# Kernel optimization log

Hardware: AMD Instinct MI355X
Metric: run time of the kernel (lower is better)

## Reference

```python
import jax, jax.numpy as jnp
import numpy as np

H = W = 256
WS = 8      # window size
SS = 4      # shift size
NH = 3      # num heads
EPS = 1e-5


def _rel_pos_index(ws):
    coords = np.stack(np.meshgrid(np.arange(ws), np.arange(ws), indexing='ij')).reshape(2, -1)
    rel = (coords[:, :, None] - coords[:, None, :]).transpose(1, 2, 0)
    rel[..., 0] += ws - 1
    rel[..., 1] += ws - 1
    rel[..., 0] *= 2 * ws - 1
    return rel.sum(-1)  # (ws*ws, ws*ws) int


def _attn_mask(h, w, ws, ss):
    img = np.zeros((h, w))
    cnt = 0
    for hs in (slice(0, -ws), slice(-ws, -ss), slice(-ss, None)):
        for wsl in (slice(0, -ws), slice(-ws, -ss), slice(-ss, None)):
            img[hs, wsl] = cnt
            cnt += 1
    mw = img.reshape(h // ws, ws, w // ws, ws).transpose(0, 2, 1, 3).reshape(-1, ws * ws)
    am = mw[:, None, :] - mw[:, :, None]
    return np.where(am != 0, -100.0, 0.0).astype(np.float32)  # (nW, N, N)


_RPI = jnp.asarray(_rel_pos_index(WS))
_MASK = jnp.asarray(_attn_mask(H, W, WS, SS))


def _ln(x, w, b):
    m = x.mean(-1, keepdims=True)
    v = ((x - m) ** 2).mean(-1, keepdims=True)
    return (x - m) * jax.lax.rsqrt(v + EPS) * w + b


def setup_inputs() -> dict:
    key = jax.random.key(0)
    ks = jax.random.split(key, 6)
    C, DFF = 96, 384
    return {
        'x': jax.random.normal(ks[0], (8, H * W, C), jnp.float32),
        'norm1_w': jnp.ones((C,), jnp.float32),
        'norm1_b': jnp.zeros((C,), jnp.float32),
        'qkv_w': jax.random.normal(ks[1], (3 * C, C), jnp.float32) * 0.02,
        'qkv_b': jnp.zeros((3 * C,), jnp.float32),
        'rpb_table': jax.random.normal(ks[2], ((2 * WS - 1) ** 2, NH), jnp.float32) * 0.02,
        'proj_w': jax.random.normal(ks[3], (C, C), jnp.float32) * 0.02,
        'proj_b': jnp.zeros((C,), jnp.float32),
        'norm2_w': jnp.ones((C,), jnp.float32),
        'norm2_b': jnp.zeros((C,), jnp.float32),
        'mlp_w1': jax.random.normal(ks[4], (DFF, C), jnp.float32) * 0.02,
        'mlp_b1': jnp.zeros((DFF,), jnp.float32),
        'mlp_w2': jax.random.normal(ks[5], (C, DFF), jnp.float32) * 0.02,
        'mlp_b2': jnp.zeros((C,), jnp.float32),
    }


def reference(x, norm1_w, norm1_b, qkv_w, qkv_b, rpb_table, proj_w, proj_b,
              norm2_w, norm2_b, mlp_w1, mlp_b1, mlp_w2, mlp_b2):
    B, L, C = x.shape
    N = WS * WS
    hd = C // NH
    scale = hd ** -0.5

    shortcut = x
    h = _ln(x, norm1_w, norm1_b).reshape(B, H, W, C)
    h = jnp.roll(h, (-SS, -SS), axis=(1, 2))
    # window partition -> (B_ , N, C)
    xw = h.reshape(B, H // WS, WS, W // WS, WS, C).transpose(0, 1, 3, 2, 4, 5).reshape(-1, N, C)
    B_ = xw.shape[0]

    qkv = (xw @ qkv_w.T + qkv_b).reshape(B_, N, 3, NH, hd).transpose(2, 0, 3, 1, 4)
    q, k, v = qkv[0], qkv[1], qkv[2]  # each (B_, NH, N, hd)
    attn = jnp.einsum('bhnd,bhmd->bhnm', q, k) * scale

    bias = rpb_table[_RPI.reshape(-1)].reshape(N, N, NH).transpose(2, 0, 1)  # (NH,N,N)
    attn = attn + bias[None]

    nW = _MASK.shape[0]
    attn = attn.reshape(B_ // nW, nW, NH, N, N) + _MASK[None, :, None]
    attn = jax.nn.softmax(attn.reshape(B_, NH, N, N), axis=-1)

    o = jnp.einsum('bhnm,bhmd->bhnd', attn, v).transpose(0, 2, 1, 3).reshape(B_, N, C)
    o = o @ proj_w.T + proj_b
    # window reverse -> (B, H, W, C)
    o = o.reshape(B, H // WS, W // WS, WS, WS, C).transpose(0, 1, 3, 2, 4, 5).reshape(B, H, W, C)
    o = jnp.roll(o, (SS, SS), axis=(1, 2))

    x1 = shortcut + o.reshape(B, L, C)
    h2 = _ln(x1, norm2_w, norm2_b)
    h2 = jax.nn.gelu(h2 @ mlp_w1.T + mlp_b1, approximate=False) @ mlp_w2.T + mlp_b2
    return x1 + h2
```

## Files before the change

kernel.cpp:

```cpp
#include <hip/hip_runtime.h>
#include <math.h>

#define HH    256
#define WWID  256
#define WSZ   8
#define SSZ   4
#define NHEAD 3
#define CCH   96
#define DFF   384

#define XW_LD 104
#define QK_LD 200
#define VT_LD 72
#define H_LD  200

using bf16x8 = __attribute__((ext_vector_type(8))) short;
using f32x4  = __attribute__((ext_vector_type(4))) float;
using int2v  = __attribute__((ext_vector_type(2))) int;

#define LOG2E 1.44269504088896f

__device__ __forceinline__ unsigned short f2bf(float f) {
    unsigned u = __float_as_uint(f);
    return (unsigned short)((u + 0x7FFFu + ((u >> 16) & 1u)) >> 16);
}
__device__ __forceinline__ float bf2f(unsigned short s) {
    return __uint_as_float(((unsigned)s) << 16);
}
__device__ __forceinline__ unsigned cvtpk(float lo, float hi) {
    unsigned r;
    asm("v_cvt_pk_bf16_f32 %0, %1, %2" : "=v"(r) : "v"(lo), "v"(hi));
    return r;
}
__device__ __forceinline__ float lo2f(unsigned u) { return __uint_as_float(u << 16); }
__device__ __forceinline__ float hi2f(unsigned u) { return __uint_as_float(u & 0xFFFF0000u); }

__device__ __forceinline__ float gelu_t(float t) {
    float t2 = t * t;
    float u  = t * (0.7978845608028654f + 0.03567740814183f * t2);
    float e  = exp2f(u * 2.885390081777927f);
    float rc = __builtin_amdgcn_rcpf(e + 1.f);
    return t - t * rc;
}

#define WQ_OFF  0
#define WP_OFF  27648
#define W1_OFF  36864
#define W2_OFF  73728
#define CT_OFF  110592

__global__ void __launch_bounds__(256)
prep(const float* __restrict__ qkvw, const float* __restrict__ pw,
     const float* __restrict__ w1, const float* __restrict__ w2,
     const float* __restrict__ rpb, unsigned short* __restrict__ wsq)
{
    int e = blockIdx.x * 256 + threadIdx.x;
    if (e < 110592) {
        const float* W; int Kd, nk, i = e;
        if (i < 27648)      { W = qkvw; Kd = 96;  nk = 3;  }
        else if (i < 36864) { W = pw;   Kd = 96;  nk = 3;  i -= 27648; }
        else if (i < 73728) { W = w1;   Kd = 96;  nk = 3;  i -= 36864; }
        else                { W = w2;   Kd = 384; nk = 12; i -= 73728; }
        int j = i & 7, fe = i >> 3;
        int lane = fe & 63, q = fe >> 6;
        int ks = q % nk, t = q / nk;
        int row = t * 16 + (lane & 15);
        int col = ks * 32 + (lane >> 4) * 8 + j;
        wsq[e] = f2bf(W[(size_t)row * Kd + col]);
    } else if (e < 159744) {
        int i = e - 110592;
        int cls = i / 12288;
        int rem = i - cls * 12288;
        int h = rem >> 12, n = (rem >> 6) & 63, m = rem & 63;
        int rel = ((n >> 3) - (m >> 3) + 7) * 15 + ((n & 7) - (m & 7) + 7);
        float bias = rpb[rel * NHEAD + h];
        int ci = cls >> 1, cj = cls & 1;
        int rn = (ci ? ((n >> 3) < 4 ? 1 : 2) : 0) * 3 + (cj ? ((n & 7) < 4 ? 1 : 2) : 0);
        int rm = (ci ? ((m >> 3) < 4 ? 1 : 2) : 0) * 3 + (cj ? ((m & 7) < 4 ? 1 : 2) : 0);
        float mask = (rn != rm) ? -100.f : 0.f;
        wsq[CT_OFF + i] = f2bf((bias + mask) * LOG2E);
    }
}

__global__ void __launch_bounds__(256, 3)
fused(const float* __restrict__ x,
      const float* __restrict__ n1w, const float* __restrict__ n1b,
      const float* __restrict__ qkvb, const float* __restrict__ pb,
      const float* __restrict__ n2w, const float* __restrict__ n2b,
      const float* __restrict__ b1, const float* __restrict__ b2,
      const unsigned short* __restrict__ wsq,
      float* __restrict__ y)
{
    __shared__ unsigned short SM[19712];
    unsigned short* sR1 = SM;
    unsigned short* sQK = SM + 6912;

    const int bwin = blockIdx.x;
    const int b  = bwin >> 10;
    const int wi = (bwin >> 5) & 31;
    const int wj = bwin & 31;
    const int tid = threadIdx.x;
    const int lane = tid & 63;
    const int wave = tid >> 6;
    const int l15 = lane & 15;
    const int l16 = lane >> 4;
    const int nb = wave * 16;
    const int sub = lane & 3;

    const int tm  = nb + (lane >> 2);
    const int gh1 = ((wi << 3) + (tm >> 3) + SSZ) & (HH - 1);
    const int gw1 = ((wj << 3) + (tm & 7) + SSZ) & (WWID - 1);
    const size_t rowtm = ((size_t)b * (HH * WWID) + (size_t)gh1 * WWID + gw1) * CCH;

    f32x4 xv[6];
    {
        const float* xr = x + rowtm + sub * 24;
#pragma unroll
        for (int q = 0; q < 6; ++q) xv[q] = *(const f32x4*)(xr + 4 * q);
        float s1 = 0.f, s2 = 0.f;
#pragma unroll
        for (int q = 0; q < 6; ++q)
#pragma unroll
            for (int r = 0; r < 4; ++r) { s1 += xv[q][r]; s2 = fmaf(xv[q][r], xv[q][r], s2); }
        s1 += __shfl_xor(s1, 1);  s2 += __shfl_xor(s2, 1);
        s1 += __shfl_xor(s1, 2);  s2 += __shfl_xor(s2, 2);
        const float mean = s1 * (1.f / CCH);
        const float rstd = rsqrtf(s2 * (1.f / CCH) - mean * mean + 1e-5f);
        unsigned o[12];
#pragma unroll
        for (int q = 0; q < 6; ++q) {
            const f32x4 wv = *(const f32x4*)&n1w[sub * 24 + 4 * q];
            const f32x4 bv = *(const f32x4*)&n1b[sub * 24 + 4 * q];
            float a0 = (xv[q][0] - mean) * rstd * wv[0] + bv[0];
            float a1 = (xv[q][1] - mean) * rstd * wv[1] + bv[1];
            float a2 = (xv[q][2] - mean) * rstd * wv[2] + bv[2];
            float a3 = (xv[q][3] - mean) * rstd * wv[3] + bv[3];
            o[2 * q] = cvtpk(a0, a1); o[2 * q + 1] = cvtpk(a2, a3);
        }
        unsigned* dst = (unsigned*)&sR1[tm * XW_LD + sub * 24];
#pragma unroll
        for (int q = 0; q < 3; ++q) {
            uint4 u; u.x = o[4 * q]; u.y = o[4 * q + 1]; u.z = o[4 * q + 2]; u.w = o[4 * q + 3];
            *(uint4*)(dst + 4 * q) = u;
        }
    }
    __syncthreads();

    bf16x8 afr[4][3];
#pragma unroll
    for (int mt = 0; mt < 4; ++mt)
#pragma unroll
        for (int ks = 0; ks < 3; ++ks)
            afr[mt][ks] = *(const bf16x8*)&sR1[(mt * 16 + l15) * XW_LD + ks * 32 + l16 * 8];
    __syncthreads();

    {
        const float qscale = 0.17677669529663689f * LOG2E;
        for (int nt = wave; nt < 18; nt += 4) {
            f32x4 acc[4] = {{0,0,0,0},{0,0,0,0},{0,0,0,0},{0,0,0,0}};
#pragma unroll
            for (int ks = 0; ks < 3; ++ks) {
                const bf16x8 wf = *(const bf16x8*)(wsq + ((size_t)(nt * 3 + ks) * 64 + lane) * 8);
#pragma unroll
                for (int mt = 0; mt < 4; ++mt)
                    acc[mt] = __builtin_amdgcn_mfma_f32_16x16x32_bf16(wf, afr[mt][ks], acc[mt], 0, 0, 0);
            }
            const f32x4 bias = *(const f32x4*)&qkvb[nt * 16 + 4 * l16];
            if (nt < 6) {
#pragma unroll
                for (int mt = 0; mt < 4; ++mt) {
                    uint2 u;
                    u.x = cvtpk((acc[mt][0] + bias[0]) * qscale, (acc[mt][1] + bias[1]) * qscale);
                    u.y = cvtpk((acc[mt][2] + bias[2]) * qscale, (acc[mt][3] + bias[3]) * qscale);
                    *(uint2*)&sQK[(mt * 16 + l15) * QK_LD + nt * 16 + 4 * l16] = u;
                }
            } else if (nt < 12) {
#pragma unroll
                for (int mt = 0; mt < 4; ++mt) {
                    uint2 u;
                    u.x = cvtpk(acc[mt][0] + bias[0], acc[mt][1] + bias[1]);
                    u.y = cvtpk(acc[mt][2] + bias[2], acc[mt][3] + bias[3]);
                    *(uint2*)&sQK[(mt * 16 + l15) * QK_LD + nt * 16 + 4 * l16] = u;
                }
            } else {
                const int ch = nt * 16 - 192 + 4 * l16;
#pragma unroll
                for (int mt = 0; mt < 4; ++mt) {
                    const unsigned v01 = cvtpk(acc[mt][0] + bias[0], acc[mt][1] + bias[1]);
                    const unsigned v23 = cvtpk(acc[mt][2] + bias[2], acc[mt][3] + bias[3]);
                    sR1[(ch + 0) * VT_LD + mt * 16 + l15] = (unsigned short)v01;
                    sR1[(ch + 1) * VT_LD + mt * 16 + l15] = (unsigned short)(v01 >> 16);
                    sR1[(ch + 2) * VT_LD + mt * 16 + l15] = (unsigned short)v23;
                    sR1[(ch + 3) * VT_LD + mt * 16 + l15] = (unsigned short)(v23 >> 16);
                }
            }
        }
    }
    __syncthreads();

    {
        const int cls = ((wi == 31) ? 2 : 0) + ((wj == 31) ? 1 : 0);
        const unsigned short* ctb = wsq + CT_OFF + cls * 12288;
        const bool godd = (l16 & 1) != 0;
#pragma unroll 1
        for (int h = 0; h < NHEAD; ++h) {
            const bf16x8 qf = *(const bf16x8*)&sQK[(nb + l15) * QK_LD + h * 32 + l16 * 8];
            f32x4 s[4];
#pragma unroll
            for (int mt = 0; mt < 4; ++mt) {
                const bf16x8 kf = *(const bf16x8*)&sQK[(mt * 16 + l15) * QK_LD + CCH + h * 32 + l16 * 8];
                f32x4 z = {0, 0, 0, 0};
                s[mt] = __builtin_amdgcn_mfma_f32_16x16x32_bf16(kf, qf, z, 0, 0, 0);
            }
            const unsigned short* cth = ctb + h * 4096 + (nb + l15) * 64;
            unsigned u[4][2];
            float rsum = 0.f;
#pragma unroll
            for (int mt = 0; mt < 4; ++mt) {
                const ushort4 c4 = *(const ushort4*)&cth[mt * 16 + 4 * l16];
                const float pv0 = exp2f(s[mt][0] + bf2f(c4.x));
                const float pv1 = exp2f(s[mt][1] + bf2f(c4.y));
                const float pv2 = exp2f(s[mt][2] + bf2f(c4.z));
                const float pv3 = exp2f(s[mt][3] + bf2f(c4.w));
                rsum += pv0 + pv1 + pv2 + pv3;
                u[mt][0] = cvtpk(pv0, pv1);
                u[mt][1] = cvtpk(pv2, pv3);
            }
            rsum += __shfl_xor(rsum, 16);
            rsum += __shfl_xor(rsum, 32);
            const float rinv = __builtin_amdgcn_rcpf(rsum);
            f32x4 o[2] = {{0,0,0,0},{0,0,0,0}};
#pragma unroll
            for (int ks = 0; ks < 2; ++ks) {
                const int2v r0 = __builtin_amdgcn_permlane32_swap(
                    (int)u[2 * ks][0], (int)u[2 * ks + 1][0], false, false);
                const int2v r1 = __builtin_amdgcn_permlane32_swap(
                    (int)u[2 * ks][1], (int)u[2 * ks + 1][1], false, false);
                const unsigned X0 = (unsigned)r0[0], Y0 = (unsigned)r0[1];
                const unsigned X1 = (unsigned)r1[0], Y1 = (unsigned)r1[1];
                const unsigned SX0 = (unsigned)__builtin_amdgcn_ds_swizzle((int)X0, 0x401F);
                const unsigned SX1 = (unsigned)__builtin_amdgcn_ds_swizzle((int)X1, 0x401F);
                const unsigned SY0 = (unsigned)__builtin_amdgcn_ds_swizzle((int)Y0, 0x401F);
                const unsigned SY1 = (unsigned)__builtin_amdgcn_ds_swizzle((int)Y1, 0x401F);
                union { unsigned w[4]; bf16x8 v; } pk;
                pk.w[0] = godd ? SY0 : X0;
                pk.w[1] = godd ? SY1 : X1;
                pk.w[2] = godd ? Y0 : SX0;
                pk.w[3] = godd ? Y1 : SX1;
#pragma unroll
                for (int dt = 0; dt < 2; ++dt) {
                    const bf16x8 vf = *(const bf16x8*)&sR1[(h * 32 + dt * 16 + l15) * VT_LD + ks * 32 + l16 * 8];
                    o[dt] = __builtin_amdgcn_mfma_f32_16x16x32_bf16(vf, pk.v, o[dt], 0, 0, 0);
                }
            }
#pragma unroll
            for (int dt = 0; dt < 2; ++dt) {
                uint2 uo;
                uo.x = cvtpk(o[dt][0] * rinv, o[dt][1] * rinv);
                uo.y = cvtpk(o[dt][2] * rinv, o[dt][3] * rinv);
                *(uint2*)&sQK[(nb + l15) * QK_LD + h * 32 + dt * 16 + 4 * l16] = uo;
            }
        }
    }
    __syncthreads();

    {
        bf16x8 ofr[4][3];
#pragma unroll
        for (int mt = 0; mt < 4; ++mt)
#pragma unroll
            for (int ks = 0; ks < 3; ++ks)
                ofr[mt][ks] = *(const bf16x8*)&sQK[(mt * 16 + l15) * QK_LD + ks * 32 + l16 * 8];
        const unsigned short* wp = wsq + WP_OFF;
        for (int ct = wave; ct < 6; ct += 4) {
            f32x4 acc[4] = {{0,0,0,0},{0,0,0,0},{0,0,0,0},{0,0,0,0}};
#pragma unroll
            for (int ks = 0; ks < 3; ++ks) {
                const bf16x8 wf = *(const bf16x8*)(wp + ((size_t)(ct * 3 + ks) * 64 + lane) * 8);
#pragma unroll
                for (int mt = 0; mt < 4; ++mt)
                    acc[mt] = __builtin_amdgcn_mfma_f32_16x16x32_bf16(wf, ofr[mt][ks], acc[mt], 0, 0, 0);
            }
            const f32x4 pbv = *(const f32x4*)&pb[ct * 16 + 4 * l16];
#pragma unroll
            for (int mt = 0; mt < 4; ++mt) {
                uint2 u;
                u.x = cvtpk(acc[mt][0] + pbv[0], acc[mt][1] + pbv[1]);
                u.y = cvtpk(acc[mt][2] + pbv[2], acc[mt][3] + pbv[3]);
                *(uint2*)&sR1[(mt * 16 + l15) * XW_LD + ct * 16 + 4 * l16] = u;
            }
        }
    }
    __syncthreads();

    float y1tm[6][4];
    {
        const unsigned* src = (const unsigned*)&sR1[tm * XW_LD + sub * 24];
#pragma unroll
        for (int q3 = 0; q3 < 3; ++q3) {
            const uint4 u = *(const uint4*)(src + 4 * q3);
            y1tm[2 * q3][0]     = xv[2 * q3][0] + lo2f(u.x);
            y1tm[2 * q3][1]     = xv[2 * q3][1] + hi2f(u.x);
            y1tm[2 * q3][2]     = xv[2 * q3][2] + lo2f(u.y);
            y1tm[2 * q3][3]     = xv[2 * q3][3] + hi2f(u.y);
            y1tm[2 * q3 + 1][0] = xv[2 * q3 + 1][0] + lo2f(u.z);
            y1tm[2 * q3 + 1][1] = xv[2 * q3 + 1][1] + hi2f(u.z);
            y1tm[2 * q3 + 1][2] = xv[2 * q3 + 1][2] + lo2f(u.w);
            y1tm[2 * q3 + 1][3] = xv[2 * q3 + 1][3] + hi2f(u.w);
        }
        float s1 = 0.f, s2 = 0.f;
#pragma unroll
        for (int q = 0; q < 6; ++q)
#pragma unroll
            for (int r = 0; r < 4; ++r) { s1 += y1tm[q][r]; s2 = fmaf(y1tm[q][r], y1tm[q][r], s2); }
        s1 += __shfl_xor(s1, 1);  s2 += __shfl_xor(s2, 1);
        s1 += __shfl_xor(s1, 2);  s2 += __shfl_xor(s2, 2);
        const float mean = s1 * (1.f / CCH);
        const float rstd = rsqrtf(s2 * (1.f / CCH) - mean * mean + 1e-5f);
        unsigned o[12];
#pragma unroll
        for (int q = 0; q < 6; ++q) {
            const f32x4 wv = *(const f32x4*)&n2w[sub * 24 + 4 * q];
            const f32x4 bv = *(const f32x4*)&n2b[sub * 24 + 4 * q];
            float a0 = (y1tm[q][0] - mean) * rstd * wv[0] + bv[0];
            float a1 = (y1tm[q][1] - mean) * rstd * wv[1] + bv[1];
            float a2 = (y1tm[q][2] - mean) * rstd * wv[2] + bv[2];
            float a3 = (y1tm[q][3] - mean) * rstd * wv[3] + bv[3];
            o[2 * q] = cvtpk(a0, a1); o[2 * q + 1] = cvtpk(a2, a3);
        }
        unsigned* dst = (unsigned*)&sR1[tm * XW_LD + sub * 24];
#pragma unroll
        for (int q = 0; q < 3; ++q) {
            uint4 u; u.x = o[4 * q]; u.y = o[4 * q + 1]; u.z = o[4 * q + 2]; u.w = o[4 * q + 3];
            *(uint4*)(dst + 4 * q) = u;
        }
    }
    __syncthreads();

    f32x4 acc2[2][4];
#pragma unroll
    for (int ci = 0; ci < 2; ++ci)
#pragma unroll
        for (int mt = 0; mt < 4; ++mt) acc2[ci][mt] = (f32x4){0, 0, 0, 0};
    const unsigned short* w2p = wsq + W2_OFF;
#pragma unroll 1
    for (int half = 0; half < 2; ++half) {
        const unsigned short* w1p = wsq + W1_OFF + (size_t)half * 12 * 3 * 64 * 8;
        for (int nt = wave; nt < 12; nt += 4) {
            f32x4 acc[4] = {{0,0,0,0},{0,0,0,0},{0,0,0,0},{0,0,0,0}};
#pragma unroll
            for (int ks = 0; ks < 3; ++ks) {
                const bf16x8 wf = *(const bf16x8*)(w1p + ((size_t)(nt * 3 + ks) * 64 + lane) * 8);
#pragma unroll
                for (int mt = 0; mt < 4; ++mt) {
                    const bf16x8 xf = *(const bf16x8*)&sR1[(mt * 16 + l15) * XW_LD + ks * 32 + l16 * 8];
                    acc[mt] = __builtin_amdgcn_mfma_f32_16x16x32_bf16(wf, xf, acc[mt], 0, 0, 0);
                }
            }
            const f32x4 b1v = *(const f32x4*)&b1[(half * 12 + nt) * 16 + 4 * l16];
#pragma unroll
            for (int mt = 0; mt < 4; ++mt) {
                uint2 u;
                u.x = cvtpk(gelu_t(acc[mt][0] + b1v[0]), gelu_t(acc[mt][1] + b1v[1]));
                u.y = cvtpk(gelu_t(acc[mt][2] + b1v[2]), gelu_t(acc[mt][3] + b1v[3]));
                *(uint2*)&sQK[(mt * 16 + l15) * H_LD + nt * 16 + 4 * l16] = u;
            }
        }
        __syncthreads();
#pragma unroll
        for (int k6 = 0; k6 < 6; ++k6) {
            bf16x8 hfr[4];
#pragma unroll
            for (int mt = 0; mt < 4; ++mt)
                hfr[mt] = *(const bf16x8*)&sQK[(mt * 16 + l15) * H_LD + k6 * 32 + l16 * 8];
#pragma unroll
            for (int ci = 0; ci < 2; ++ci) {
                const int ct = wave + 4 * ci;
                if (ct < 6) {
                    const bf16x8 wf = *(const bf16x8*)(w2p + ((size_t)(ct * 12 + half * 6 + k6) * 64 + lane) * 8);
#pragma unroll
                    for (int mt = 0; mt < 4; ++mt)
                        acc2[ci][mt] = __builtin_amdgcn_mfma_f32_16x16x32_bf16(wf, hfr[mt], acc2[ci][mt], 0, 0, 0);
                }
            }
        }
        if (half == 0) __syncthreads();
    }

    {
#pragma unroll
        for (int ci = 0; ci < 2; ++ci) {
            const int ct = wave + 4 * ci;
            if (ct < 6) {
                const f32x4 b2v = *(const f32x4*)&b2[ct * 16 + 4 * l16];
#pragma unroll
                for (int mt = 0; mt < 4; ++mt) {
                    uint2 u;
                    u.x = cvtpk(acc2[ci][mt][0] + b2v[0], acc2[ci][mt][1] + b2v[1]);
                    u.y = cvtpk(acc2[ci][mt][2] + b2v[2], acc2[ci][mt][3] + b2v[3]);
                    *(uint2*)&sR1[(mt * 16 + l15) * XW_LD + ct * 16 + 4 * l16] = u;
                }
            }
        }
    }
    __syncthreads();
    {
        const unsigned* src = (const unsigned*)&sR1[tm * XW_LD + sub * 24];
        float* yr = y + rowtm + sub * 24;
#pragma unroll
        for (int q3 = 0; q3 < 3; ++q3) {
            const uint4 u = *(const uint4*)(src + 4 * q3);
            f32x4 o0, o1;
            o0[0] = y1tm[2 * q3][0] + lo2f(u.x);
            o0[1] = y1tm[2 * q3][1] + hi2f(u.x);
            o0[2] = y1tm[2 * q3][2] + lo2f(u.y);
            o0[3] = y1tm[2 * q3][3] + hi2f(u.y);
            o1[0] = y1tm[2 * q3 + 1][0] + lo2f(u.z);
            o1[1] = y1tm[2 * q3 + 1][1] + hi2f(u.z);
            o1[2] = y1tm[2 * q3 + 1][2] + lo2f(u.w);
            o1[3] = y1tm[2 * q3 + 1][3] + hi2f(u.w);
            *(f32x4*)(yr + 8 * q3)     = o0;
            *(f32x4*)(yr + 8 * q3 + 4) = o1;
        }
    }
}

extern "C" void kernel_launch(void* const* d_in, const int* in_sizes, int n_in,
                              void* d_out, int out_size, void* d_ws, size_t ws_size,
                              hipStream_t stream)
{
    const float* x    = (const float*)d_in[0];
    const float* n1w  = (const float*)d_in[1];
    const float* n1b  = (const float*)d_in[2];
    const float* qkvw = (const float*)d_in[3];
    const float* qkvb = (const float*)d_in[4];
    const float* rpb  = (const float*)d_in[5];
    const float* pw   = (const float*)d_in[6];
    const float* pb   = (const float*)d_in[7];
    const float* n2w  = (const float*)d_in[8];
    const float* n2b  = (const float*)d_in[9];
    const float* w1   = (const float*)d_in[10];
    const float* b1   = (const float*)d_in[11];
    const float* w2   = (const float*)d_in[12];
    const float* b2   = (const float*)d_in[13];
    float* out = (float*)d_out;

    unsigned short* wsq = (unsigned short*)d_ws;

    prep<<<dim3(624), dim3(256), 0, stream>>>(qkvw, pw, w1, w2, rpb, wsq);
    fused<<<dim3(8192), dim3(256), 0, stream>>>(x, n1w, n1b, qkvb, pb, n2w, n2b,
                                                b1, b2, wsq, out);
}
```

Baseline: 318.6 us.

## Repartition MLP second GEMM by token rows per wave and raise occupancy to 4

The second MLP GEMM is reorganized so each wave owns one 16-token row block (nb) and computes all six output column tiles. Before, waves split the output by column tile, which left waves 2-3 with only one of two tiles active. The change balances the work across waves and cuts the accumulator registers from 8 f32x4 to 6. It also lets launch_bounds request 4 blocks per CU instead of 3. The cost is that every wave now streams all of the W2 weight fragments from global memory, and a tighter register cap could cause spills elsewhere in the kernel.

```diff
diff --git a/kernel.cpp b/kernel.cpp
--- a/kernel.cpp
+++ b/kernel.cpp
@@ -82,7 +82,7 @@
     }
 }
 
-__global__ void __launch_bounds__(256, 3)
+__global__ void __launch_bounds__(256, 4)
 fused(const float* __restrict__ x,
       const float* __restrict__ n1w, const float* __restrict__ n1b,
       const float* __restrict__ qkvb, const float* __restrict__ pb,
@@ -337,11 +337,9 @@
     }
     __syncthreads();
 
-    f32x4 acc2[2][4];
-#pragma unroll
-    for (int ci = 0; ci < 2; ++ci)
-#pragma unroll
-        for (int mt = 0; mt < 4; ++mt) acc2[ci][mt] = (f32x4){0, 0, 0, 0};
+    f32x4 acc2[6];
+#pragma unroll
+    for (int ct = 0; ct < 6; ++ct) acc2[ct] = (f32x4){0, 0, 0, 0};
     const unsigned short* w2p = wsq + W2_OFF;
 #pragma unroll 1
     for (int half = 0; half < 2; ++half) {
@@ -369,19 +367,11 @@
         __syncthreads();
 #pragma unroll
         for (int k6 = 0; k6 < 6; ++k6) {
-            bf16x8 hfr[4];
-#pragma unroll
-            for (int mt = 0; mt < 4; ++mt)
-                hfr[mt] = *(const bf16x8*)&sQK[(mt * 16 + l15) * H_LD + k6 * 32 + l16 * 8];
-#pragma unroll
-            for (int ci = 0; ci < 2; ++ci) {
-                const int ct = wave + 4 * ci;
-                if (ct < 6) {
-                    const bf16x8 wf = *(const bf16x8*)(w2p + ((size_t)(ct * 12 + half * 6 + k6) * 64 + lane) * 8);
-#pragma unroll
-                    for (int mt = 0; mt < 4; ++mt)
-                        acc2[ci][mt] = __builtin_amdgcn_mfma_f32_16x16x32_bf16(wf, hfr[mt], acc2[ci][mt], 0, 0, 0);
-                }
+            const bf16x8 hfr = *(const bf16x8*)&sQK[(nb + l15) * H_LD + k6 * 32 + l16 * 8];
+#pragma unroll
+            for (int ct = 0; ct < 6; ++ct) {
+                const bf16x8 wf = *(const bf16x8*)(w2p + ((size_t)(ct * 12 + half * 6 + k6) * 64 + lane) * 8);
+                acc2[ct] = __builtin_amdgcn_mfma_f32_16x16x32_bf16(wf, hfr, acc2[ct], 0, 0, 0);
             }
         }
         if (half == 0) __syncthreads();
@@ -389,18 +379,12 @@
 
     {
 #pragma unroll
-        for (int ci = 0; ci < 2; ++ci) {
-            const int ct = wave + 4 * ci;
-            if (ct < 6) {
-                const f32x4 b2v = *(const f32x4*)&b2[ct * 16 + 4 * l16];
-#pragma unroll
-                for (int mt = 0; mt < 4; ++mt) {
-                    uint2 u;
-                    u.x = cvtpk(acc2[ci][mt][0] + b2v[0], acc2[ci][mt][1] + b2v[1]);
-                    u.y = cvtpk(acc2[ci][mt][2] + b2v[2], acc2[ci][mt][3] + b2v[3]);
-                    *(uint2*)&sR1[(mt * 16 + l15) * XW_LD + ct * 16 + 4 * l16] = u;
-                }
-            }
+        for (int ct = 0; ct < 6; ++ct) {
+            const f32x4 b2v = *(const f32x4*)&b2[ct * 16 + 4 * l16];
+            uint2 u;
+            u.x = cvtpk(acc2[ct][0] + b2v[0], acc2[ct][1] + b2v[1]);
+            u.y = cvtpk(acc2[ct][2] + b2v[2], acc2[ct][3] + b2v[3]);
+            *(uint2*)&sR1[(nb + l15) * XW_LD + ct * 16 + 4 * l16] = u;
         }
     }
     __syncthreads();
```

Result: no change. 323.6 us (+1.6%).

## Keep attention output in registers and fuse projection per wave

Applied to the files above, without the earlier changes.

The attention output for each head is transposed in registers with permlane/swizzle shuffles into MFMA B-operand fragments, instead of being written to shared memory and read back after a barrier. Each wave then computes the output projection for its own 16 tokens across all 6 column tiles, rather than splitting column tiles across waves over all 64 tokens. This removes one __syncthreads and a shared-memory round trip, and it evens out the projection work, which was previously unbalanced (6 tiles over 4 waves). In exchange it adds register pressure and extra cross-lane shuffles, and each wave now loads all projection weights itself.

```diff
diff --git a/kernel.cpp b/kernel.cpp
--- a/kernel.cpp
+++ b/kernel.cpp
@@ -41,6 +41,24 @@
     float e  = exp2f(u * 2.885390081777927f);
     float rc = __builtin_amdgcn_rcpf(e + 1.f);
     return t - t * rc;
+}
+
+__device__ __forceinline__ bf16x8 xpose_pair(unsigned a0, unsigned a1,
+                                             unsigned b0, unsigned b1, bool godd) {
+    const int2v r0 = __builtin_amdgcn_permlane32_swap((int)a0, (int)b0, false, false);
+    const int2v r1 = __builtin_amdgcn_permlane32_swap((int)a1, (int)b1, false, false);
+    const unsigned X0 = (unsigned)r0[0], Y0 = (unsigned)r0[1];
+    const unsigned X1 = (unsigned)r1[0], Y1 = (unsigned)r1[1];
+    const unsigned SX0 = (unsigned)__builtin_amdgcn_ds_swizzle((int)X0, 0x401F);
+    const unsigned SX1 = (unsigned)__builtin_amdgcn_ds_swizzle((int)X1, 0x401F);
+    const unsigned SY0 = (unsigned)__builtin_amdgcn_ds_swizzle((int)Y0, 0x401F);
+    const unsigned SY1 = (unsigned)__builtin_amdgcn_ds_swizzle((int)Y1, 0x401F);
+    union { unsigned w[4]; bf16x8 v; } pk;
+    pk.w[0] = godd ? SY0 : X0;
+    pk.w[1] = godd ? SY1 : X1;
+    pk.w[2] = godd ? Y0 : SX0;
+    pk.w[3] = godd ? Y1 : SX1;
+    return pk.v;
 }
 
 #define WQ_OFF  0
@@ -106,6 +124,7 @@
     const int l16 = lane >> 4;
     const int nb = wave * 16;
     const int sub = lane & 3;
+    const bool godd = (l16 & 1) != 0;
 
     const int tm  = nb + (lane >> 2);
     const int gh1 = ((wi << 3) + (tm >> 3) + SSZ) & (HH - 1);
@@ -201,7 +220,7 @@
     {
         const int cls = ((wi == 31) ? 2 : 0) + ((wj == 31) ? 1 : 0);
         const unsigned short* ctb = wsq + CT_OFF + cls * 12288;
-        const bool godd = (l16 & 1) != 0;
+        bf16x8 pofr[3];
 #pragma unroll 1
         for (int h = 0; h < NHEAD; ++h) {
             const bf16x8 qf = *(const bf16x8*)&sQK[(nb + l15) * QK_LD + h * 32 + l16 * 8];
@@ -232,70 +251,41 @@
             f32x4 o[2] = {{0,0,0,0},{0,0,0,0}};
 #pragma unroll
             for (int ks = 0; ks < 2; ++ks) {
-                const int2v r0 = __builtin_amdgcn_permlane32_swap(
-                    (int)u[2 * ks][0], (int)u[2 * ks + 1][0], false, false);
-                const int2v r1 = __builtin_amdgcn_permlane32_swap(
-                    (int)u[2 * ks][1], (int)u[2 * ks + 1][1], false, false);
-                const unsigned X0 = (unsigned)r0[0], Y0 = (unsigned)r0[1];
-                const unsigned X1 = (unsigned)r1[0], Y1 = (unsigned)r1[1];
-                const unsigned SX0 = (unsigned)__builtin_amdgcn_ds_swizzle((int)X0, 0x401F);
-                const unsigned SX1 = (unsigned)__builtin_amdgcn_ds_swizzle((int)X1, 0x401F);
-                const unsigned SY0 = (unsigned)__builtin_amdgcn_ds_swizzle((int)Y0, 0x401F);
-                const unsigned SY1 = (unsigned)__builtin_amdgcn_ds_swizzle((int)Y1, 0x401F);
-                union { unsigned w[4]; bf16x8 v; } pk;
-                pk.w[0] = godd ? SY0 : X0;
-                pk.w[1] = godd ? SY1 : X1;
-                pk.w[2] = godd ? Y0 : SX0;
-                pk.w[3] = godd ? Y1 : SX1;
+                const bf16x8 pk = xpose_pair(u[2 * ks][0], u[2 * ks][1],
+                                             u[2 * ks + 1][0], u[2 * ks + 1][1], godd);
 #pragma unroll
                 for (int dt = 0; dt < 2; ++dt) {
                     const bf16x8 vf = *(const bf16x8*)&sR1[(h * 32 + dt * 16 + l15) * VT_LD + ks * 32 + l16 * 8];
-                    o[dt] = __builtin_amdgcn_mfma_f32_16x16x32_bf16(vf, pk.v, o[dt], 0, 0, 0);
-                }
-            }
-#pragma unroll
-            for (int dt = 0; dt < 2; ++dt) {
-                uint2 uo;
-                uo.x = cvtpk(o[dt][0] * rinv, o[dt][1] * rinv);
-                uo.y = cvtpk(o[dt][2] * rinv, o[dt][3] * rinv);
-                *(uint2*)&sQK[(nb + l15) * QK_LD + h * 32 + dt * 16 + 4 * l16] = uo;
-            }
-        }
-    }
-    __syncthreads();
-
-    {
-        bf16x8 ofr[4][3];
-#pragma unroll
-        for (int mt = 0; mt < 4; ++mt)
-#pragma unroll
-            for (int ks = 0; ks < 3; ++ks)
-                ofr[mt][ks] = *(const bf16x8*)&sQK[(mt * 16 + l15) * QK_LD + ks * 32 + l16 * 8];
+                    o[dt] = __builtin_amdgcn_mfma_f32_16x16x32_bf16(vf, pk, o[dt], 0, 0, 0);
+                }
+            }
+            const unsigned uo00 = cvtpk(o[0][0] * rinv, o[0][1] * rinv);
+            const unsigned uo01 = cvtpk(o[0][2] * rinv, o[0][3] * rinv);
+            const unsigned uo10 = cvtpk(o[1][0] * rinv, o[1][1] * rinv);
+            const unsigned uo11 = cvtpk(o[1][2] * rinv, o[1][3] * rinv);
+            pofr[h] = xpose_pair(uo00, uo01, uo10, uo11, godd);
+        }
         const unsigned short* wp = wsq + WP_OFF;
-        for (int ct = wave; ct < 6; ct += 4) {
-            f32x4 acc[4] = {{0,0,0,0},{0,0,0,0},{0,0,0,0},{0,0,0,0}};
+#pragma unroll
+        for (int ct = 0; ct < 6; ++ct) {
+            f32x4 acc = {0, 0, 0, 0};
 #pragma unroll
             for (int ks = 0; ks < 3; ++ks) {
                 const bf16x8 wf = *(const bf16x8*)(wp + ((size_t)(ct * 3 + ks) * 64 + lane) * 8);
-#pragma unroll
-                for (int mt = 0; mt < 4; ++mt)
-                    acc[mt] = __builtin_amdgcn_mfma_f32_16x16x32_bf16(wf, ofr[mt][ks], acc[mt], 0, 0, 0);
+                acc = __builtin_amdgcn_mfma_f32_16x16x32_bf16(wf, pofr[ks], acc, 0, 0, 0);
             }
             const f32x4 pbv = *(const f32x4*)&pb[ct * 16 + 4 * l16];
-#pragma unroll
-            for (int mt = 0; mt < 4; ++mt) {
-                uint2 u;
-                u.x = cvtpk(acc[mt][0] + pbv[0], acc[mt][1] + pbv[1]);
-                u.y = cvtpk(acc[mt][2] + pbv[2], acc[mt][3] + pbv[3]);
-                *(uint2*)&sR1[(mt * 16 + l15) * XW_LD + ct * 16 + 4 * l16] = u;
-            }
+            uint2 u;
+            u.x = cvtpk(acc[0] + pbv[0], acc[1] + pbv[1]);
+            u.y = cvtpk(acc[2] + pbv[2], acc[3] + pbv[3]);
+            *(uint2*)&sQK[(nb + l15) * QK_LD + ct * 16 + 4 * l16] = u;
         }
     }
     __syncthreads();
 
     float y1tm[6][4];
     {
-        const unsigned* src = (const unsigned*)&sR1[tm * XW_LD + sub * 24];
+        const unsigned* src = (const unsigned*)&sQK[tm * QK_LD + sub * 24];
 #pragma unroll
         for (int q3 = 0; q3 < 3; ++q3) {
             const uint4 u = *(const uint4*)(src + 4 * q3);
```

New measurement: 342.8 us. 7.6% more time.
